# Optimization experiments

Measured on AMD Instinct MI355X. Metric: run time of the kernel, lower is better.

## Reference

```python
import jax, jax.numpy as jnp
import numpy as np

N = 65536
LAYER_DIMS = [(3, 3), (3, 20), (20, 20), (20, 20), (20, 20), (20, 20), (20, 20), (20, 2)]


def setup_inputs() -> dict:
    key = jax.random.key(0)
    ks = jax.random.split(key, 1 + 2 * len(LAYER_DIMS))
    inp = {"X": jax.random.uniform(ks[0], (N, 3), dtype=jnp.float32)}
    for i, (din, dout) in enumerate(LAYER_DIMS):
        inp[f"W{i+1}"] = jax.random.normal(ks[1 + 2 * i], (din, dout), dtype=jnp.float32) / np.float32(np.sqrt(din))
        inp[f"b{i+1}"] = jnp.zeros((dout,), dtype=jnp.float32)
    inp["lam1"] = jnp.array([1.0], dtype=jnp.float32)
    inp["lam2"] = jnp.array([0.01], dtype=jnp.float32)
    return inp


def _forward(X, Ws, bs, lam1, lam2):
    # lb/ub from the x-coordinate; computed outside the tapes in the original,
    # so they are constants w.r.t. differentiation.
    lb = jax.lax.stop_gradient(jnp.min(X[:, 0]))
    ub = jax.lax.stop_gradient(jnp.max(X[:, 0]))

    def net(xi):  # xi: [3] -> [2] (psi, p)
        h = 2.0 * (xi - lb) / (ub - lb) - 1.0
        for W, b in zip(Ws, bs):
            h = jnp.tanh(h @ W + b)
        return h

    psi_fn = lambda xi: net(xi)[0]
    p_fn = lambda xi: net(xi)[1]

    def per_point(xi):
        p_val = net(xi)[1]
        g_psi = jax.grad(psi_fn)(xi)            # [3]
        u = g_psi[1]
        v = -g_psi[0]
        g_p = jax.grad(p_fn)(xi)                # [3]
        p_x, p_y = g_p[0], g_p[1]
        Hs = jax.hessian(psi_fn)(xi)            # [3,3]
        u_x, u_y, u_t = Hs[1, 0], Hs[1, 1], Hs[1, 2]
        v_x, v_y, v_t = -Hs[0, 0], -Hs[0, 1], -Hs[0, 2]
        T = jax.jacfwd(jax.hessian(psi_fn))(xi)  # [3,3,3] third derivs of psi
        u_xx, u_yy = T[1, 0, 0], T[1, 1, 1]
        v_xx, v_yy = -T[0, 0, 0], -T[0, 1, 1]
        return (u, v, p_val, p_x, p_y, u_t, u_x, u_y, v_t, v_x, v_y, u_xx, u_yy, v_xx, v_yy)

    (u, v, p_val, p_x, p_y, u_t, u_x, u_y, v_t, v_x, v_y,
     u_xx, u_yy, v_xx, v_yy) = jax.vmap(per_point)(X)

    f_u = u_t + lam1 * (u * u_x + v * u_y) + p_x - lam2 * (u_xx + u_yy)
    f_v = v_t + lam1 * (u * v_x + v * v_y) + p_y - lam2 * (v_xx + v_yy)
    return (u, v, p_val[:, None], f_u, f_v)


def reference(X, W1, b1, W2, b2, W3, b3, W4, b4, W5, b5, W6, b6, W7, b7, W8, b8, lam1, lam2):
    Ws = [W1, W2, W3, W4, W5, W6, W7, W8]
    bs = [b1, b2, b3, b4, b5, b6, b7, b8]
    return _forward(X, Ws, bs, lam1, lam2)
```

## Files before the change

### kernel.cpp

```cpp
#include <hip/hip_runtime.h>

#define NPTS 65536
#define MM_BLOCKS 64

__device__ __forceinline__ float fast_tanh(float x) {
  float e = __expf(2.0f * x);
  float r = __builtin_amdgcn_rcpf(e + 1.0f);
  return fmaf(-2.0f, r, 1.0f);
}

template <int M> __device__ __forceinline__ constexpr int qpctrl() {
  return M == 1 ? 0xB1 : (M == 2 ? 0x4E : 0x1B);
}
template <int M> __device__ __forceinline__ float qperm(float x) {
  return __int_as_float(__builtin_amdgcn_mov_dpp(
      __float_as_int(x), qpctrl<M>(), 0xF, 0xF, true));
}

struct J3 {
  float v, c1, c2, c3;
  __device__ __forceinline__ static J3 seed(float bias) {
    J3 z; z.v = bias; z.c1 = 0.f; z.c2 = 0.f; z.c3 = 0.f; return z;
  }
  __device__ __forceinline__ void macc(float w, const J3& o) {
    v  = fmaf(w, o.v,  v);
    c1 = fmaf(w, o.c1, c1);
    c2 = fmaf(w, o.c2, c2);
    c3 = fmaf(w, o.c3, c3);
  }
  __device__ __forceinline__ J3 chain() const {
    float s    = fast_tanh(v);
    float fp   = fmaf(-s, s, 1.0f);
    float fpp  = -2.0f * s * fp;
    float fppp = fmaf(6.0f * s, s, -2.0f) * fp;
    J3 r;
    r.v  = s;
    r.c1 = fp * c1;
    r.c2 = fmaf(fpp, c1 * c1, fp * c2);
    r.c3 = fmaf(fppp * c1, c1 * c1, fmaf(3.0f * fpp, c1 * c2, fp * c3));
    return r;
  }
};

struct J3t {
  float v, c1, c2, c3, t, m;
  __device__ __forceinline__ static J3t seed(float bias) {
    J3t z; z.v = bias; z.c1 = 0.f; z.c2 = 0.f; z.c3 = 0.f; z.t = 0.f; z.m = 0.f;
    return z;
  }
  __device__ __forceinline__ void macc(float w, const J3t& o) {
    v  = fmaf(w, o.v,  v);
    c1 = fmaf(w, o.c1, c1);
    c2 = fmaf(w, o.c2, c2);
    c3 = fmaf(w, o.c3, c3);
    t  = fmaf(w, o.t,  t);
    m  = fmaf(w, o.m,  m);
  }
  __device__ __forceinline__ J3t chain() const {
    float s    = fast_tanh(v);
    float fp   = fmaf(-s, s, 1.0f);
    float fpp  = -2.0f * s * fp;
    float fppp = fmaf(6.0f * s, s, -2.0f) * fp;
    J3t r;
    r.v  = s;
    r.c1 = fp * c1;
    r.c2 = fmaf(fpp, c1 * c1, fp * c2);
    r.c3 = fmaf(fppp * c1, c1 * c1, fmaf(3.0f * fpp, c1 * c2, fp * c3));
    r.t  = fp * t;
    r.m  = fmaf(fpp, c1 * t, fp * m);
    return r;
  }
};

template <int M> __device__ __forceinline__ J3 shflx(const J3& o) {
  J3 r;
  r.v  = qperm<M>(o.v);
  r.c1 = qperm<M>(o.c1);
  r.c2 = qperm<M>(o.c2);
  r.c3 = qperm<M>(o.c3);
  return r;
}
template <int M> __device__ __forceinline__ J3t shflx(const J3t& o) {
  J3t r;
  r.v  = qperm<M>(o.v);
  r.c1 = qperm<M>(o.c1);
  r.c2 = qperm<M>(o.c2);
  r.c3 = qperm<M>(o.c3);
  r.t  = qperm<M>(o.t);
  r.m  = qperm<M>(o.m);
  return r;
}
template <int M> __device__ __forceinline__ void redsum(J3& z) {
  z.v  += qperm<M>(z.v);
  z.c1 += qperm<M>(z.c1);
  z.c2 += qperm<M>(z.c2);
  z.c3 += qperm<M>(z.c3);
}
template <int M> __device__ __forceinline__ void redsum(J3t& z) {
  z.v  += qperm<M>(z.v);
  z.c1 += qperm<M>(z.c1);
  z.c2 += qperm<M>(z.c2);
  z.c3 += qperm<M>(z.c3);
  z.t  += qperm<M>(z.t);
  z.m  += qperm<M>(z.m);
}

template <class J>
__device__ __forceinline__ void layer20_q(const float* __restrict__ W,
                                          const float* __restrict__ bias,
                                          int hb, int hb1, int hb2, int hb3,
                                          const J* A, J* B) {
  const float* B0 = W + hb  * 20 + hb;
  const float* B1 = W + hb1 * 20 + hb;
  const float* B2 = W + hb2 * 20 + hb;
  const float* B3 = W + hb3 * 20 + hb;
#pragma unroll
  for (int j = 0; j < 5; ++j) B[j] = J::seed(bias[hb + j]);
#pragma unroll
  for (int ii = 0; ii < 5; ++ii) {
    J s = A[ii];
#pragma unroll
    for (int j = 0; j < 5; ++j) B[j].macc(B0[ii * 20 + j], s);
    s = shflx<1>(A[ii]);
#pragma unroll
    for (int j = 0; j < 5; ++j) B[j].macc(B1[ii * 20 + j], s);
    s = shflx<2>(A[ii]);
#pragma unroll
    for (int j = 0; j < 5; ++j) B[j].macc(B2[ii * 20 + j], s);
    s = shflx<3>(A[ii]);
#pragma unroll
    for (int j = 0; j < 5; ++j) B[j].macc(B3[ii * 20 + j], s);
  }
#pragma unroll
  for (int j = 0; j < 5; ++j) B[j] = B[j].chain();
}

#define LDS_W_FLOATS 2234

template <class J, bool WANTP>
__device__ __forceinline__ void run_net(const float* __restrict__ w,
                                        int hb, int hb1, int hb2, int hb3,
                                        const J* in3, J& Opsi, J& Op) {
  J A[5], B[5];
  {
    J T[3];
#pragma unroll
    for (int j = 0; j < 3; ++j) {
      J z = J::seed(w[9 + j]);
#pragma unroll
      for (int i = 0; i < 3; ++i) z.macc(w[i * 3 + j], in3[i]);
      T[j] = z.chain();
    }
#pragma unroll
    for (int j = 0; j < 5; ++j) {
      J z = J::seed(w[72 + hb + j]);
#pragma unroll
      for (int i = 0; i < 3; ++i) z.macc(w[12 + i * 20 + hb + j], T[i]);
      A[j] = z.chain();
    }
  }
#pragma unroll 1
  for (int l = 0; l < 5; ++l) {
    const float* Wl = w + 92 + l * 420;
    layer20_q(Wl, Wl + 400, hb, hb1, hb2, hb3, A, B);
#pragma unroll
    for (int jj = 0; jj < 5; ++jj) A[jj] = B[jj];
  }
  J z0 = J::seed(0.f);
#pragma unroll
  for (int ii = 0; ii < 5; ++ii) z0.macc(w[2192 + (hb + ii) * 2 + 0], A[ii]);
  redsum<1>(z0); redsum<2>(z0);
  z0.v += w[2232];
  Opsi = z0.chain();
  if constexpr (WANTP) {
    J z1 = J::seed(0.f);
#pragma unroll
    for (int ii = 0; ii < 5; ++ii) z1.macc(w[2192 + (hb + ii) * 2 + 1], A[ii]);
    redsum<1>(z1); redsum<2>(z1);
    z1.v += w[2233];
    Op = z1.chain();
  }
}

__device__ __forceinline__ unsigned flipk(float f) {
  unsigned u = __float_as_uint(f);
  return (u & 0x80000000u) ? ~u : (u | 0x80000000u);
}
__device__ __forceinline__ float unflip(unsigned k) {
  unsigned u = (k & 0x80000000u) ? (k ^ 0x80000000u) : ~k;
  return __uint_as_float(u);
}

__global__ void __launch_bounds__(256) mm_reduce(const float* __restrict__ X,
                                                 unsigned* __restrict__ mm) {
  __shared__ unsigned smin[4], smax[4];
  unsigned kmin = 0xFFFFFFFFu, kmax = 0u;
  for (int i = blockIdx.x * 256 + threadIdx.x; i < NPTS; i += gridDim.x * 256) {
    unsigned key = flipk(X[3 * i]);
    kmin = min(kmin, key);
    kmax = max(kmax, key);
  }
#pragma unroll
  for (int o = 32; o > 0; o >>= 1) {
    kmin = min(kmin, (unsigned)__shfl_down((int)kmin, o, 64));
    kmax = max(kmax, (unsigned)__shfl_down((int)kmax, o, 64));
  }
  int wv = threadIdx.x >> 6;
  if ((threadIdx.x & 63) == 0) { smin[wv] = kmin; smax[wv] = kmax; }
  __syncthreads();
  if (threadIdx.x == 0) {
    kmin = min(min(smin[0], smin[1]), min(smin[2], smin[3]));
    kmax = max(max(smax[0], smax[1]), max(smax[2], smax[3]));
    mm[2 * blockIdx.x + 0] = kmin;
    mm[2 * blockIdx.x + 1] = kmax;
  }
}

__global__ void __launch_bounds__(256, 2) pinn_main(
    const float* __restrict__ X,
    const float* W1, const float* b1, const float* W2, const float* b2,
    const float* W3, const float* b3, const float* W4, const float* b4,
    const float* W5, const float* b5, const float* W6, const float* b6,
    const float* W7, const float* b7, const float* W8, const float* b8,
    const float* lam1p, const float* lam2p, const unsigned* __restrict__ mm,
    float* __restrict__ out) {
  __shared__ float w[LDS_W_FLOATS];
  {
    const float* Wsrc[8] = {W1, W2, W3, W4, W5, W6, W7, W8};
    const float* bsrc[8] = {b1, b2, b3, b4, b5, b6, b7, b8};
    const int nwA[8]  = {9, 60, 400, 400, 400, 400, 400, 40};
    const int nbA[8]  = {3, 20, 20, 20, 20, 20, 20, 2};
    const int offW[8] = {0, 12, 92, 512, 932, 1352, 1772, 2192};
    const int offB[8] = {9, 72, 492, 912, 1332, 1752, 2172, 2232};
#pragma unroll
    for (int a = 0; a < 8; ++a) {
      for (int s = threadIdx.x; s < nwA[a]; s += 256) w[offW[a] + s] = Wsrc[a][s];
      for (int s = threadIdx.x; s < nbA[a]; s += 256) w[offB[a] + s] = bsrc[a][s];
    }
  }

  const int lane = threadIdx.x & 63;
  const int gid  = blockIdx.x * 256 + threadIdx.x;
  const int pt   = gid >> 3;
  const int Q    = gid & 3;
  const int q    = (gid >> 2) & 1;
  const int hb   = 5 * Q;
  const int hb1  = 5 * (Q ^ 1);
  const int hb2  = 5 * (Q ^ 2);
  const int hb3  = 5 * (Q ^ 3);

  unsigned pmin = mm[2 * lane + 0];
  unsigned pmax = mm[2 * lane + 1];
#pragma unroll
  for (int o = 1; o < 64; o <<= 1) {
    pmin = min(pmin, (unsigned)__shfl_xor((int)pmin, o, 64));
    pmax = max(pmax, (unsigned)__shfl_xor((int)pmax, o, 64));
  }
  float lb = unflip(pmin);
  float ub = unflip(pmax);
  float kk = 2.0f / (ub - lb);

  float x = X[3 * pt], y = X[3 * pt + 1], tt = X[3 * pt + 2];
  float h0 = fmaf(kk, x - lb, -1.0f);
  float h1 = fmaf(kk, y - lb, -1.0f);
  float h2 = fmaf(kk, tt - lb, -1.0f);

  __syncthreads();

  float a0 = q ? 0.0f : kk, a1 = q ? kk : 0.0f;
  float b1s = q ? -kk : kk;

  float rc1, rc2, rc3, rpv, rpc;
  float s2, s3, rm;

  {
    J3 I[3], Opsi, Op;
    I[0].v = h0; I[0].c1 = a0;  I[0].c2 = 0.f; I[0].c3 = 0.f;
    I[1].v = h1; I[1].c1 = a1;  I[1].c2 = 0.f; I[1].c3 = 0.f;
    I[2].v = h2; I[2].c1 = 0.f; I[2].c2 = 0.f; I[2].c3 = 0.f;
    run_net<J3, true>(w, hb, hb1, hb2, hb3, I, Opsi, Op);
    rc1 = Opsi.c1; rc2 = Opsi.c2; rc3 = Opsi.c3;
    rpv = Op.v;    rpc = Op.c1;
  }
  {
    J3t I[3], Opsi, Odummy;
    I[0].v = h0; I[0].c1 = kk;  I[0].c2 = 0.f; I[0].c3 = 0.f; I[0].t = 0.f; I[0].m = 0.f;
    I[1].v = h1; I[1].c1 = b1s; I[1].c2 = 0.f; I[1].c3 = 0.f; I[1].t = 0.f; I[1].m = 0.f;
    I[2].v = h2; I[2].c1 = 0.f; I[2].c2 = 0.f; I[2].c3 = 0.f; I[2].t = kk;  I[2].m = 0.f;
    run_net<J3t, false>(w, hb, hb1, hb2, hb3, I, Opsi, Odummy);
    s2 = Opsi.c2; s3 = Opsi.c3; rm = Opsi.m;
  }

  float psi_y   = __shfl_xor(rc1, 4, 64);
  float psi_yy  = __shfl_xor(rc2, 4, 64);
  float psi_yyy = __shfl_xor(rc3, 4, 64);
  float p_y     = __shfl_xor(rpc, 4, 64);
  float S2m     = __shfl_xor(s2, 4, 64);
  float S3m     = __shfl_xor(s3, 4, 64);
  float mB      = __shfl_xor(rm, 4, 64);

  if ((gid & 7) == 0) {
    float psi_x = rc1, psi_xx = rc2, psi_xxx = rc3;
    float p_val = rpv, p_x = rpc;
    float S2p = s2, S3p = s3;

    float psi_xy  = 0.25f * (S2p - S2m);
    float psi_xxy = (S3p - S3m - 2.0f * psi_yyy) * (1.0f / 6.0f);
    float psi_xyy = (S3p + S3m - 2.0f * psi_xxx) * (1.0f / 6.0f);
    float psi_xt  = 0.5f * (rm + mB);
    float psi_yt  = 0.5f * (rm - mB);

    float u = psi_y, vv = -psi_x;
    float u_x = psi_xy,  u_y = psi_yy,  u_t = psi_yt;
    float v_x = -psi_xx, v_y = -psi_xy, v_t = -psi_xt;
    float u_xx = psi_xxy,  u_yy = psi_yyy;
    float v_xx = -psi_xxx, v_yy = -psi_xyy;

    float lam1 = lam1p[0], lam2 = lam2p[0];
    float f_u = u_t + lam1 * (u * u_x + vv * u_y) + p_x - lam2 * (u_xx + u_yy);
    float f_v = v_t + lam1 * (u * v_x + vv * v_y) + p_y - lam2 * (v_xx + v_yy);

    out[pt] = u;
    out[NPTS + pt] = vv;
    out[2 * NPTS + pt] = p_val;
    out[3 * NPTS + pt] = f_u;
    out[4 * NPTS + pt] = f_v;
  }
}

extern "C" void kernel_launch(void* const* d_in, const int* in_sizes, int n_in,
                              void* d_out, int out_size, void* d_ws, size_t ws_size,
                              hipStream_t stream) {
  (void)in_sizes; (void)n_in; (void)out_size; (void)ws_size;
  const float* X = (const float*)d_in[0];
  const float* W[8]; const float* B[8];
  for (int i = 0; i < 8; ++i) {
    W[i] = (const float*)d_in[1 + 2 * i];
    B[i] = (const float*)d_in[2 + 2 * i];
  }
  const float* lam1 = (const float*)d_in[17];
  const float* lam2 = (const float*)d_in[18];
  unsigned* mm = (unsigned*)d_ws;
  float* out = (float*)d_out;

  hipLaunchKernelGGL(mm_reduce, dim3(MM_BLOCKS), dim3(256), 0, stream, X, mm);
  hipLaunchKernelGGL(pinn_main, dim3(8 * NPTS / 256), dim3(256), 0, stream,
                     X, W[0], B[0], W[1], B[1], W[2], B[2], W[3], B[3],
                     W[4], B[4], W[5], B[5], W[6], B[6], W[7], B[7],
                     lam1, lam2, mm, out);
}
```

Baseline: 205.4 us.

## Fuse two network passes into a single nine-component jet propagation

Replaces the two separate forward passes (a 4-component jet and a 6-component jet) with one pass carrying a 9-component jet that shares the primal value and the tanh evaluation. This removes the duplicated primal propagation, the duplicated tanh and derivative computation, and half of the weight loads and DPP shuffles of the primal. The cost is that each lane now holds 9 floats per neuron for 10 neurons, so register pressure rises and occupancy may drop. The p output head is reduced to a scalar first-order computation.

```diff
diff --git a/kernel.cpp b/kernel.cpp
--- a/kernel.cpp
+++ b/kernel.cpp
@@ -17,108 +17,83 @@
       __float_as_int(x), qpctrl<M>(), 0xF, 0xF, true));
 }
 
-struct J3 {
-  float v, c1, c2, c3;
-  __device__ __forceinline__ static J3 seed(float bias) {
-    J3 z; z.v = bias; z.c1 = 0.f; z.c2 = 0.f; z.c3 = 0.f; return z;
-  }
-  __device__ __forceinline__ void macc(float w, const J3& o) {
+struct J9 {
+  float v, a1, a2, a3, b1, b2, b3, t, m;
+  __device__ __forceinline__ static J9 seed(float bias) {
+    J9 z; z.v = bias;
+    z.a1 = 0.f; z.a2 = 0.f; z.a3 = 0.f;
+    z.b1 = 0.f; z.b2 = 0.f; z.b3 = 0.f;
+    z.t = 0.f; z.m = 0.f;
+    return z;
+  }
+  __device__ __forceinline__ void macc(float w, const J9& o) {
     v  = fmaf(w, o.v,  v);
-    c1 = fmaf(w, o.c1, c1);
-    c2 = fmaf(w, o.c2, c2);
-    c3 = fmaf(w, o.c3, c3);
-  }
-  __device__ __forceinline__ J3 chain() const {
+    a1 = fmaf(w, o.a1, a1);
+    a2 = fmaf(w, o.a2, a2);
+    a3 = fmaf(w, o.a3, a3);
+    b1 = fmaf(w, o.b1, b1);
+    b2 = fmaf(w, o.b2, b2);
+    b3 = fmaf(w, o.b3, b3);
+    t  = fmaf(w, o.t,  t);
+    m  = fmaf(w, o.m,  m);
+  }
+  __device__ __forceinline__ J9 chain() const {
     float s    = fast_tanh(v);
     float fp   = fmaf(-s, s, 1.0f);
     float fpp  = -2.0f * s * fp;
     float fppp = fmaf(6.0f * s, s, -2.0f) * fp;
-    J3 r;
+    J9 r;
     r.v  = s;
-    r.c1 = fp * c1;
-    r.c2 = fmaf(fpp, c1 * c1, fp * c2);
-    r.c3 = fmaf(fppp * c1, c1 * c1, fmaf(3.0f * fpp, c1 * c2, fp * c3));
+    r.a1 = fp * a1;
+    r.a2 = fmaf(fpp, a1 * a1, fp * a2);
+    r.a3 = fmaf(fppp * a1, a1 * a1, fmaf(3.0f * fpp, a1 * a2, fp * a3));
+    r.b1 = fp * b1;
+    r.b2 = fmaf(fpp, b1 * b1, fp * b2);
+    r.b3 = fmaf(fppp * b1, b1 * b1, fmaf(3.0f * fpp, b1 * b2, fp * b3));
+    r.t  = fp * t;
+    r.m  = fmaf(fpp, b1 * t, fp * m);
     return r;
   }
 };
 
-struct J3t {
-  float v, c1, c2, c3, t, m;
-  __device__ __forceinline__ static J3t seed(float bias) {
-    J3t z; z.v = bias; z.c1 = 0.f; z.c2 = 0.f; z.c3 = 0.f; z.t = 0.f; z.m = 0.f;
-    return z;
-  }
-  __device__ __forceinline__ void macc(float w, const J3t& o) {
-    v  = fmaf(w, o.v,  v);
-    c1 = fmaf(w, o.c1, c1);
-    c2 = fmaf(w, o.c2, c2);
-    c3 = fmaf(w, o.c3, c3);
-    t  = fmaf(w, o.t,  t);
-    m  = fmaf(w, o.m,  m);
-  }
-  __device__ __forceinline__ J3t chain() const {
-    float s    = fast_tanh(v);
-    float fp   = fmaf(-s, s, 1.0f);
-    float fpp  = -2.0f * s * fp;
-    float fppp = fmaf(6.0f * s, s, -2.0f) * fp;
-    J3t r;
-    r.v  = s;
-    r.c1 = fp * c1;
-    r.c2 = fmaf(fpp, c1 * c1, fp * c2);
-    r.c3 = fmaf(fppp * c1, c1 * c1, fmaf(3.0f * fpp, c1 * c2, fp * c3));
-    r.t  = fp * t;
-    r.m  = fmaf(fpp, c1 * t, fp * m);
-    return r;
-  }
-};
-
-template <int M> __device__ __forceinline__ J3 shflx(const J3& o) {
-  J3 r;
+template <int M> __device__ __forceinline__ J9 shflx(const J9& o) {
+  J9 r;
   r.v  = qperm<M>(o.v);
-  r.c1 = qperm<M>(o.c1);
-  r.c2 = qperm<M>(o.c2);
-  r.c3 = qperm<M>(o.c3);
-  return r;
-}
-template <int M> __device__ __forceinline__ J3t shflx(const J3t& o) {
-  J3t r;
-  r.v  = qperm<M>(o.v);
-  r.c1 = qperm<M>(o.c1);
-  r.c2 = qperm<M>(o.c2);
-  r.c3 = qperm<M>(o.c3);
+  r.a1 = qperm<M>(o.a1);
+  r.a2 = qperm<M>(o.a2);
+  r.a3 = qperm<M>(o.a3);
+  r.b1 = qperm<M>(o.b1);
+  r.b2 = qperm<M>(o.b2);
+  r.b3 = qperm<M>(o.b3);
   r.t  = qperm<M>(o.t);
   r.m  = qperm<M>(o.m);
   return r;
 }
-template <int M> __device__ __forceinline__ void redsum(J3& z) {
+template <int M> __device__ __forceinline__ void redsum(J9& z) {
   z.v  += qperm<M>(z.v);
-  z.c1 += qperm<M>(z.c1);
-  z.c2 += qperm<M>(z.c2);
-  z.c3 += qperm<M>(z.c3);
-}
-template <int M> __device__ __forceinline__ void redsum(J3t& z) {
-  z.v  += qperm<M>(z.v);
-  z.c1 += qperm<M>(z.c1);
-  z.c2 += qperm<M>(z.c2);
-  z.c3 += qperm<M>(z.c3);
+  z.a1 += qperm<M>(z.a1);
+  z.a2 += qperm<M>(z.a2);
+  z.a3 += qperm<M>(z.a3);
+  z.b1 += qperm<M>(z.b1);
+  z.b2 += qperm<M>(z.b2);
+  z.b3 += qperm<M>(z.b3);
   z.t  += qperm<M>(z.t);
   z.m  += qperm<M>(z.m);
 }
 
-template <class J>
 __device__ __forceinline__ void layer20_q(const float* __restrict__ W,
                                           const float* __restrict__ bias,
                                           int hb, int hb1, int hb2, int hb3,
-                                          const J* A, J* B) {
+                                          const J9* A, J9* B) {
   const float* B0 = W + hb  * 20 + hb;
   const float* B1 = W + hb1 * 20 + hb;
   const float* B2 = W + hb2 * 20 + hb;
   const float* B3 = W + hb3 * 20 + hb;
 #pragma unroll
-  for (int j = 0; j < 5; ++j) B[j] = J::seed(bias[hb + j]);
+  for (int j = 0; j < 5; ++j) B[j] = J9::seed(bias[hb + j]);
 #pragma unroll
   for (int ii = 0; ii < 5; ++ii) {
-    J s = A[ii];
+    J9 s = A[ii];
 #pragma unroll
     for (int j = 0; j < 5; ++j) B[j].macc(B0[ii * 20 + j], s);
     s = shflx<1>(A[ii]);
@@ -136,51 +111,6 @@
 }
 
 #define LDS_W_FLOATS 2234
-
-template <class J, bool WANTP>
-__device__ __forceinline__ void run_net(const float* __restrict__ w,
-                                        int hb, int hb1, int hb2, int hb3,
-                                        const J* in3, J& Opsi, J& Op) {
-  J A[5], B[5];
-  {
-    J T[3];
-#pragma unroll
-    for (int j = 0; j < 3; ++j) {
-      J z = J::seed(w[9 + j]);
-#pragma unroll
-      for (int i = 0; i < 3; ++i) z.macc(w[i * 3 + j], in3[i]);
-      T[j] = z.chain();
-    }
-#pragma unroll
-    for (int j = 0; j < 5; ++j) {
-      J z = J::seed(w[72 + hb + j]);
-#pragma unroll
-      for (int i = 0; i < 3; ++i) z.macc(w[12 + i * 20 + hb + j], T[i]);
-      A[j] = z.chain();
-    }
-  }
-#pragma unroll 1
-  for (int l = 0; l < 5; ++l) {
-    const float* Wl = w + 92 + l * 420;
-    layer20_q(Wl, Wl + 400, hb, hb1, hb2, hb3, A, B);
-#pragma unroll
-    for (int jj = 0; jj < 5; ++jj) A[jj] = B[jj];
-  }
-  J z0 = J::seed(0.f);
-#pragma unroll
-  for (int ii = 0; ii < 5; ++ii) z0.macc(w[2192 + (hb + ii) * 2 + 0], A[ii]);
-  redsum<1>(z0); redsum<2>(z0);
-  z0.v += w[2232];
-  Opsi = z0.chain();
-  if constexpr (WANTP) {
-    J z1 = J::seed(0.f);
-#pragma unroll
-    for (int ii = 0; ii < 5; ++ii) z1.macc(w[2192 + (hb + ii) * 2 + 1], A[ii]);
-    redsum<1>(z1); redsum<2>(z1);
-    z1.v += w[2233];
-    Op = z1.chain();
-  }
-}
 
 __device__ __forceinline__ unsigned flipk(float f) {
   unsigned u = __float_as_uint(f);
@@ -267,28 +197,68 @@
 
   __syncthreads();
 
-  float a0 = q ? 0.0f : kk, a1 = q ? kk : 0.0f;
+  float a0s = q ? 0.0f : kk, a1s = q ? kk : 0.0f;
   float b1s = q ? -kk : kk;
 
-  float rc1, rc2, rc3, rpv, rpc;
-  float s2, s3, rm;
-
+  J9 A[5], B[5];
   {
-    J3 I[3], Opsi, Op;
-    I[0].v = h0; I[0].c1 = a0;  I[0].c2 = 0.f; I[0].c3 = 0.f;
-    I[1].v = h1; I[1].c1 = a1;  I[1].c2 = 0.f; I[1].c3 = 0.f;
-    I[2].v = h2; I[2].c1 = 0.f; I[2].c2 = 0.f; I[2].c3 = 0.f;
-    run_net<J3, true>(w, hb, hb1, hb2, hb3, I, Opsi, Op);
-    rc1 = Opsi.c1; rc2 = Opsi.c2; rc3 = Opsi.c3;
-    rpv = Op.v;    rpc = Op.c1;
-  }
+    J9 T[3];
+    {
+      J9 I0 = J9::seed(0.f), I1 = J9::seed(0.f), I2 = J9::seed(0.f);
+      I0.v = h0; I0.a1 = a0s; I0.b1 = kk;
+      I1.v = h1; I1.a1 = a1s; I1.b1 = b1s;
+      I2.v = h2; I2.t = kk;
+#pragma unroll
+      for (int j = 0; j < 3; ++j) {
+        J9 z = J9::seed(w[9 + j]);
+        z.macc(w[0 * 3 + j], I0);
+        z.macc(w[1 * 3 + j], I1);
+        z.macc(w[2 * 3 + j], I2);
+        T[j] = z.chain();
+      }
+    }
+#pragma unroll
+    for (int j = 0; j < 5; ++j) {
+      J9 z = J9::seed(w[72 + hb + j]);
+#pragma unroll
+      for (int i = 0; i < 3; ++i) z.macc(w[12 + i * 20 + hb + j], T[i]);
+      A[j] = z.chain();
+    }
+  }
+#pragma unroll 1
+  for (int l = 0; l < 5; ++l) {
+    const float* Wl = w + 92 + l * 420;
+    layer20_q(Wl, Wl + 400, hb, hb1, hb2, hb3, A, B);
+#pragma unroll
+    for (int jj = 0; jj < 5; ++jj) A[jj] = B[jj];
+  }
+
+  float rc1, rc2, rc3, s2, s3, rm;
   {
-    J3t I[3], Opsi, Odummy;
-    I[0].v = h0; I[0].c1 = kk;  I[0].c2 = 0.f; I[0].c3 = 0.f; I[0].t = 0.f; I[0].m = 0.f;
-    I[1].v = h1; I[1].c1 = b1s; I[1].c2 = 0.f; I[1].c3 = 0.f; I[1].t = 0.f; I[1].m = 0.f;
-    I[2].v = h2; I[2].c1 = 0.f; I[2].c2 = 0.f; I[2].c3 = 0.f; I[2].t = kk;  I[2].m = 0.f;
-    run_net<J3t, false>(w, hb, hb1, hb2, hb3, I, Opsi, Odummy);
-    s2 = Opsi.c2; s3 = Opsi.c3; rm = Opsi.m;
+    J9 z = J9::seed(0.f);
+#pragma unroll
+    for (int ii = 0; ii < 5; ++ii) z.macc(w[2192 + (hb + ii) * 2 + 0], A[ii]);
+    redsum<1>(z); redsum<2>(z);
+    z.v += w[2232];
+    J9 o = z.chain();
+    rc1 = o.a1; rc2 = o.a2; rc3 = o.a3;
+    s2 = o.b2; s3 = o.b3; rm = o.m;
+  }
+  float rpv, rpc;
+  {
+    float pv = 0.f, pa = 0.f;
+#pragma unroll
+    for (int ii = 0; ii < 5; ++ii) {
+      float wt = w[2192 + (hb + ii) * 2 + 1];
+      pv = fmaf(wt, A[ii].v,  pv);
+      pa = fmaf(wt, A[ii].a1, pa);
+    }
+    pv += qperm<1>(pv); pa += qperm<1>(pa);
+    pv += qperm<2>(pv); pa += qperm<2>(pa);
+    pv += w[2233];
+    float s = fast_tanh(pv);
+    rpv = s;
+    rpc = fmaf(-s, s, 1.0f) * pa;
   }
 
   float psi_y   = __shfl_xor(rc1, 4, 64);
```

Measured after the change: 181.5 us (median of 2 runs). 1.13x faster.
